# Performance work log

Measured on AMD Instinct MI355X. Metric: run time of the kernel, lower is better.

The kernel has to match this reference:

```python
import jax, jax.numpy as jnp
import numpy as np

MESH_SIZE = 0.01
TEMP = 0.001
T = 4096
HID = (16, 16, 16)


def _triangle_mesh():
    g = np.arange(-1.0, 1.0 + 1e-9, MESH_SIZE, dtype=np.float32)  # 201 pts
    A, B = np.meshgrid(g, g, indexing='ij')  # alpha rows, beta cols
    mask = A >= B                             # Preisach triangle alpha >= beta
    return A[mask].astype(np.float32), B[mask].astype(np.float32)  # [N], [N]


def _constrain(v, lo, hi):
    return lo + (hi - lo) * jax.nn.sigmoid(v)


def setup_inputs() -> dict:
    key = jax.random.key(0)
    ks = jax.random.split(key, 12)
    alpha_np, beta_np = _triangle_mesh()
    N = alpha_np.shape[0]  # 20301

    def xavier(k, fan_in, fan_out):
        b = np.sqrt(6.0 / (fan_in + fan_out)).astype(np.float32)
        return jax.random.uniform(k, (fan_in, fan_out), jnp.float32, -b, b)

    dims = (2,) + HID + (1,)
    params = {}
    for i in range(4):
        params[f'w{i+1}'] = xavier(ks[i], dims[i], dims[i + 1])
        params[f'b{i+1}'] = jnp.zeros((dims[i + 1],), jnp.float32)

    bound = np.sqrt(6.0 / (1 + N)).astype(np.float32)  # xavier_uniform on (1,N)
    init_state_raw = jax.random.uniform(ks[10], (N,), jnp.float32, -bound, bound)

    return dict(
        x=jax.random.normal(ks[11], (T,), jnp.float32),
        alpha_raw=jnp.asarray(alpha_np),
        beta_raw=jnp.asarray(beta_np),
        init_state_raw=init_state_raw,
        m_scale_raw=jnp.asarray(1.0, jnp.float32),
        m_offset_raw=jnp.asarray(1.0, jnp.float32),
        h_scale_raw=jnp.asarray(1.0, jnp.float32),
        **params,
    )


def _get_states(x, alpha, beta, s0, temp):
    # Soft Preisach relay: switch up where u>alpha, down where u<beta, else hold.
    def step(s, u):
        up = jax.nn.sigmoid((u - alpha) / temp)
        dn = jax.nn.sigmoid((beta - u) / temp)
        s_new = up - dn + (1.0 - up) * (1.0 - dn) * s
        return s_new, s_new
    _, states = jax.lax.scan(step, s0, x)
    return states  # [T, N]


def reference(x, alpha_raw, beta_raw, init_state_raw,
              w1, b1, w2, b2, w3, b3, w4, b4,
              m_scale_raw, m_offset_raw, h_scale_raw):
    alpha = alpha_raw  # ConstrainedParameter with no bounds -> identity
    beta = beta_raw
    s0 = jnp.tanh(init_state_raw)  # BinaryParameter (soft binary)

    states = _get_states(x, alpha, beta, s0, TEMP)  # [T, N]

    mesh = jnp.stack([alpha, beta], axis=1)  # [N, 2]
    h = jax.nn.relu(mesh @ w1 + b1)
    h = jax.nn.relu(h @ w2 + b2)
    h = jax.nn.relu(h @ w3 + b3)
    density = jax.nn.sigmoid(h @ w4 + b4)  # [N, 1]
    density = density.T  # [1, N]

    m = jnp.sum(density * states, axis=-1) / jnp.sum(density, axis=-1)  # [T]

    m_scale = _constrain(m_scale_raw, 0.0, 10.0)
    m_offset = _constrain(m_offset_raw, -10.0, 10.0)
    h_scale = _constrain(h_scale_raw, 0.0, 10.0)

    out = m_scale * m + m_offset + h_scale * x  # [T]
    return out, density, states
```

## Files before the change

### kernel.cpp

```cpp
#include <hip/hip_runtime.h>
#include <math.h>

#define NM 20301
#define TT 4096
#define NC 16
#define CH 256
#define NBLK 80
#define NWAVE 4
#define NPAR (NBLK*NWAVE)
#define TPH 16
#define NPH (CH / TPH)
#define LOG2E_K 1442.69504f

__device__ __forceinline__ void relay_step(float ka, float kb, float ku,
                                           float& aa, float& bb) {
    float z1 = fminf(ka - ku, 63.f);
    float z2 = fminf(ku - kb, 63.f);
    float e1 = __builtin_amdgcn_exp2f(z1);
    float e2 = __builtin_amdgcn_exp2f(z2);
    float p1 = 1.f + e1, p2 = 1.f + e2;
    float r  = __builtin_amdgcn_rcpf(p1 * p2);
    aa = (e2 - e1) * r;
    bb = (e1 * e2) * r;
}

__device__ __forceinline__ float wave_reduce_sum(float w) {
    #pragma unroll
    for (int off = 32; off > 0; off >>= 1)
        w += __shfl_down(w, off, 64);
    return w;
}

__global__ __launch_bounds__(256) void density_kernel(
    const float* __restrict__ alpha, const float* __restrict__ beta,
    const float* __restrict__ w1, const float* __restrict__ b1,
    const float* __restrict__ w2, const float* __restrict__ b2,
    const float* __restrict__ w3, const float* __restrict__ b3,
    const float* __restrict__ w4, const float* __restrict__ b4,
    float* __restrict__ density_out, float* __restrict__ densum_parts)
{
    int n = blockIdx.x * 256 + threadIdx.x;
    bool valid = n < NM;
    int nn = valid ? n : NM - 1;
    float a = alpha[nn], b = beta[nn];

    float h1[16], h2[16], h3[16];
    #pragma unroll
    for (int j = 0; j < 16; j++) {
        float v = fmaf(a, w1[j], fmaf(b, w1[16 + j], b1[j]));
        h1[j] = fmaxf(v, 0.f);
    }
    #pragma unroll
    for (int j = 0; j < 16; j++) {
        float v = b2[j];
        #pragma unroll
        for (int k = 0; k < 16; k++) v = fmaf(h1[k], w2[k * 16 + j], v);
        h2[j] = fmaxf(v, 0.f);
    }
    #pragma unroll
    for (int j = 0; j < 16; j++) {
        float v = b3[j];
        #pragma unroll
        for (int k = 0; k < 16; k++) v = fmaf(h2[k], w3[k * 16 + j], v);
        h3[j] = fmaxf(v, 0.f);
    }
    float v = b4[0];
    #pragma unroll
    for (int k = 0; k < 16; k++) v = fmaf(h3[k], w4[k], v);
    float d = 1.f / (1.f + __expf(-v));

    if (valid) density_out[n] = d;
    float wsum = wave_reduce_sum(valid ? d : 0.f);
    __shared__ float ws_[NWAVE];
    if ((threadIdx.x & 63) == 0) ws_[threadIdx.x >> 6] = wsum;
    __syncthreads();
    if (threadIdx.x == 0)
        densum_parts[blockIdx.x] = ws_[0] + ws_[1] + ws_[2] + ws_[3];
}

__global__ __launch_bounds__(256) void chunk_compose_kernel(
    const float* __restrict__ x, const float* __restrict__ alpha,
    const float* __restrict__ beta,
    float* __restrict__ Abuf, float* __restrict__ Bbuf)
{
    __shared__ float xs[CH];
    int c = blockIdx.y;
    xs[threadIdx.x] = x[c * CH + threadIdx.x] * LOG2E_K;
    __syncthreads();

    int n = blockIdx.x * 256 + threadIdx.x;
    int nn = (n < NM) ? n : NM - 1;
    float ka = alpha[nn] * LOG2E_K;
    float kb = beta[nn] * LOG2E_K;

    float A = 0.f, B = 1.f;
    #pragma unroll 8
    for (int i = 0; i < CH; i++) {
        float aa, bb;
        relay_step(ka, kb, xs[i], aa, bb);
        A = fmaf(bb, A, aa);
        B *= bb;
    }
    if (n < NM) { Abuf[c * NM + n] = A; Bbuf[c * NM + n] = B; }
}

__global__ __launch_bounds__(256) void chunk_scan_kernel(
    const float* __restrict__ init_raw,
    const float* __restrict__ Abuf, const float* __restrict__ Bbuf,
    float* __restrict__ sstart)
{
    int n = blockIdx.x * 256 + threadIdx.x;
    if (n >= NM) return;
    float s = tanhf(init_raw[n]);
    #pragma unroll
    for (int c = 0; c < NC; c++) {
        sstart[c * NM + n] = s;
        s = fmaf(Bbuf[c * NM + n], s, Abuf[c * NM + n]);
    }
}

__global__ __launch_bounds__(256) void states_kernel(
    const float* __restrict__ x, const float* __restrict__ alpha,
    const float* __restrict__ beta, const float* __restrict__ density,
    const float* __restrict__ sstart,
    float* __restrict__ states, float* __restrict__ partials)
{
    __shared__ float xs[CH];
    __shared__ float tile[NWAVE * 64 * (TPH + 1)];

    int tid = threadIdx.x;
    int c = blockIdx.y;
    xs[tid] = x[c * CH + tid] * LOG2E_K;

    int n = blockIdx.x * 256 + tid;
    bool valid = n < NM;
    int nn = valid ? n : NM - 1;
    float ka = alpha[nn] * LOG2E_K;
    float kb = beta[nn] * LOG2E_K;
    float d  = valid ? density[n] : 0.f;
    float s  = sstart[c * NM + nn];
    __syncthreads();

    int wv = tid >> 6, ln = tid & 63;
    int tl = ln & 15, h = ln >> 4;
    float* wtile = &tile[wv * 64 * (TPH + 1)];
    float* tslot = &wtile[ln * (TPH + 1)];
    float* rowp  = states + (size_t)c * CH * NM + n;
    size_t prow  = (size_t)(blockIdx.x * NWAVE + wv) * TT + c * CH;

    for (int p = 0; p < NPH; p++) {
        #pragma unroll
        for (int j = 0; j < TPH; j++) {
            int i = p * TPH + j;
            float aa, bb;
            relay_step(ka, kb, xs[i], aa, bb);
            s = fmaf(bb, s, aa);
            if (valid) __builtin_nontemporal_store(s, rowp + (size_t)i * NM);
            tslot[j] = d * s;
        }
        asm volatile("s_waitcnt lgkmcnt(0)" ::: "memory");
        float acc = 0.f;
        #pragma unroll
        for (int k = 0; k < TPH; k++)
            acc += wtile[(h * 16 + k) * (TPH + 1) + tl];
        acc += __shfl_xor(acc, 16, 64);
        acc += __shfl_xor(acc, 32, 64);
        if (ln < TPH) partials[prow + p * TPH + ln] = acc;
        asm volatile("s_waitcnt lgkmcnt(0)" ::: "memory");
    }
}

__global__ __launch_bounds__(256) void finalize_kernel(
    const float* __restrict__ x, const float* __restrict__ partials,
    const float* __restrict__ densum_parts,
    const float* __restrict__ msr, const float* __restrict__ mor,
    const float* __restrict__ hsr, float* __restrict__ out)
{
    int t = blockIdx.x * 256 + threadIdx.x;
    if (t >= TT) return;
    float acc = 0.f;
    for (int r = 0; r < NPAR; r++)
        acc += partials[(size_t)r * TT + t];
    float dsum = 0.f;
    for (int bx = 0; bx < NBLK; bx++)
        dsum += densum_parts[bx];
    float sig_ms = 1.f / (1.f + __expf(-msr[0]));
    float sig_mo = 1.f / (1.f + __expf(-mor[0]));
    float sig_hs = 1.f / (1.f + __expf(-hsr[0]));
    float m_scale  = 10.f * sig_ms;
    float m_offset = fmaf(20.f, sig_mo, -10.f);
    float h_scale  = 10.f * sig_hs;
    float m = acc / dsum;
    out[t] = fmaf(m_scale, m, m_offset) + h_scale * x[t];
}

extern "C" void kernel_launch(void* const* d_in, const int* in_sizes, int n_in,
                              void* d_out, int out_size, void* d_ws, size_t ws_size,
                              hipStream_t stream)
{
    const float* x    = (const float*)d_in[0];
    const float* alpha= (const float*)d_in[1];
    const float* beta = (const float*)d_in[2];
    const float* init = (const float*)d_in[3];
    const float* msr  = (const float*)d_in[4];
    const float* mor  = (const float*)d_in[5];
    const float* hsr  = (const float*)d_in[6];
    const float* w1   = (const float*)d_in[7];
    const float* b1   = (const float*)d_in[8];
    const float* w2   = (const float*)d_in[9];
    const float* b2   = (const float*)d_in[10];
    const float* w3   = (const float*)d_in[11];
    const float* b3   = (const float*)d_in[12];
    const float* w4   = (const float*)d_in[13];
    const float* b4   = (const float*)d_in[14];

    float* out     = (float*)d_out;
    float* density = out + TT;
    float* states  = density + NM;

    float* densum_parts = (float*)d_ws;
    float* sstart       = densum_parts + 128;
    float* partials     = sstart + NC * NM;

    float* Abuf = states;
    float* Bbuf = states + (size_t)NC * NM;

    density_kernel<<<dim3(NBLK), dim3(256), 0, stream>>>(
        alpha, beta, w1, b1, w2, b2, w3, b3, w4, b4, density, densum_parts);

    chunk_compose_kernel<<<dim3(NBLK, NC), dim3(256), 0, stream>>>(
        x, alpha, beta, Abuf, Bbuf);

    chunk_scan_kernel<<<dim3(NBLK), dim3(256), 0, stream>>>(
        init, Abuf, Bbuf, sstart);

    states_kernel<<<dim3(NBLK, NC), dim3(256), 0, stream>>>(
        x, alpha, beta, density, sstart, states, partials);

    finalize_kernel<<<dim3(TT / 256), dim3(256), 0, stream>>>(
        x, partials, densum_parts, msr, mor, hsr, out);
}
```

Baseline: 512.4 us.

## Fuse pipeline into cooperative mega-kernel with saturated-relay fast path

Replaces the five launches with one cooperative kernel that uses grid.sync between phases: density MLP plus chunk composition, then states with an inline chunk-prefix scan, then the final reduction. Adds a wave-uniform branch that skips the exp/rcp relay math when every lane's input is far from both thresholds, setting the saturated value directly. Also drops the nontemporal stores and switches to 64-wide per-wave tasks with 8-step partial sums. It removes launch overhead and transcendental work, at the cost of grid-sync overhead, the redundant prefix recompute and a branch that only pays off when inputs are often saturated.

```diff
diff --git a/kernel.cpp b/kernel.cpp
--- a/kernel.cpp
+++ b/kernel.cpp
@@ -1,16 +1,20 @@
 #include <hip/hip_runtime.h>
+#include <hip/hip_cooperative_groups.h>
 #include <math.h>
+
+namespace cg = cooperative_groups;
 
 #define NM 20301
 #define TT 4096
 #define NC 16
 #define CH 256
-#define NBLK 80
-#define NWAVE 4
-#define NPAR (NBLK*NWAVE)
-#define TPH 16
-#define NPH (CH / TPH)
+#define NW 318
+#define NMP (NW * 64)
+#define NTASK (NW * NC)
+#define NBLOCKS 256
+#define NTH 1024
 #define LOG2E_K 1442.69504f
+#define WNEAR 26.0f
 
 __device__ __forceinline__ void relay_step(float ka, float kb, float ku,
                                            float& aa, float& bb) {
@@ -31,167 +35,167 @@
     return w;
 }
 
-__global__ __launch_bounds__(256) void density_kernel(
-    const float* __restrict__ alpha, const float* __restrict__ beta,
+__global__ __launch_bounds__(NTH, 4) void mega_kernel(
+    const float* __restrict__ x, const float* __restrict__ alpha,
+    const float* __restrict__ beta, const float* __restrict__ init_raw,
+    const float* __restrict__ msr, const float* __restrict__ mor,
+    const float* __restrict__ hsr,
     const float* __restrict__ w1, const float* __restrict__ b1,
     const float* __restrict__ w2, const float* __restrict__ b2,
     const float* __restrict__ w3, const float* __restrict__ b3,
     const float* __restrict__ w4, const float* __restrict__ b4,
-    float* __restrict__ density_out, float* __restrict__ densum_parts)
+    float* __restrict__ out, float* __restrict__ density,
+    float* __restrict__ states,
+    float* __restrict__ Ag, float* __restrict__ Bg,
+    float* __restrict__ wpart, float* __restrict__ s0g,
+    float* __restrict__ dparts)
 {
-    int n = blockIdx.x * 256 + threadIdx.x;
-    bool valid = n < NM;
-    int nn = valid ? n : NM - 1;
-    float a = alpha[nn], b = beta[nn];
-
-    float h1[16], h2[16], h3[16];
+    __shared__ float xall[TT];
+    __shared__ float tiles[16 * 64 * 9];
+
+    cg::grid_group grid = cg::this_grid();
+    int b = blockIdx.x, tid = threadIdx.x;
+    int ln = tid & 63, wv = tid >> 6;
+    int g = b * NTH + tid;
+
+    for (int q = tid; q < TT; q += NTH) xall[q] = x[q] * LOG2E_K;
+    __syncthreads();
+
+    if (g < NMP) {
+        bool valid = g < NM;
+        int nn = valid ? g : NM - 1;
+        float a = alpha[nn], bb_ = beta[nn];
+        float h1[16], h2[16], h3[16];
+        #pragma unroll
+        for (int j = 0; j < 16; j++) {
+            float v = fmaf(a, w1[j], fmaf(bb_, w1[16 + j], b1[j]));
+            h1[j] = fmaxf(v, 0.f);
+        }
+        #pragma unroll
+        for (int j = 0; j < 16; j++) {
+            float v = b2[j];
+            #pragma unroll
+            for (int k = 0; k < 16; k++) v = fmaf(h1[k], w2[k * 16 + j], v);
+            h2[j] = fmaxf(v, 0.f);
+        }
+        #pragma unroll
+        for (int j = 0; j < 16; j++) {
+            float v = b3[j];
+            #pragma unroll
+            for (int k = 0; k < 16; k++) v = fmaf(h2[k], w3[k * 16 + j], v);
+            h3[j] = fmaxf(v, 0.f);
+        }
+        float v = b4[0];
+        #pragma unroll
+        for (int k = 0; k < 16; k++) v = fmaf(h3[k], w4[k], v);
+        float d = 1.f / (1.f + __expf(-v));
+        if (valid) { density[g] = d; s0g[g] = tanhf(init_raw[g]); }
+        float wsum = wave_reduce_sum(valid ? d : 0.f);
+        if (ln == 0) dparts[g >> 6] = wsum;
+    }
+
     #pragma unroll
-    for (int j = 0; j < 16; j++) {
-        float v = fmaf(a, w1[j], fmaf(b, w1[16 + j], b1[j]));
-        h1[j] = fmaxf(v, 0.f);
-    }
-    #pragma unroll
-    for (int j = 0; j < 16; j++) {
-        float v = b2[j];
-        #pragma unroll
-        for (int k = 0; k < 16; k++) v = fmaf(h1[k], w2[k * 16 + j], v);
-        h2[j] = fmaxf(v, 0.f);
-    }
-    #pragma unroll
-    for (int j = 0; j < 16; j++) {
-        float v = b3[j];
-        #pragma unroll
-        for (int k = 0; k < 16; k++) v = fmaf(h2[k], w3[k * 16 + j], v);
-        h3[j] = fmaxf(v, 0.f);
-    }
-    float v = b4[0];
-    #pragma unroll
-    for (int k = 0; k < 16; k++) v = fmaf(h3[k], w4[k], v);
-    float d = 1.f / (1.f + __expf(-v));
-
-    if (valid) density_out[n] = d;
-    float wsum = wave_reduce_sum(valid ? d : 0.f);
-    __shared__ float ws_[NWAVE];
-    if ((threadIdx.x & 63) == 0) ws_[threadIdx.x >> 6] = wsum;
-    __syncthreads();
-    if (threadIdx.x == 0)
-        densum_parts[blockIdx.x] = ws_[0] + ws_[1] + ws_[2] + ws_[3];
-}
-
-__global__ __launch_bounds__(256) void chunk_compose_kernel(
-    const float* __restrict__ x, const float* __restrict__ alpha,
-    const float* __restrict__ beta,
-    float* __restrict__ Abuf, float* __restrict__ Bbuf)
-{
-    __shared__ float xs[CH];
-    int c = blockIdx.y;
-    xs[threadIdx.x] = x[c * CH + threadIdx.x] * LOG2E_K;
-    __syncthreads();
-
-    int n = blockIdx.x * 256 + threadIdx.x;
-    int nn = (n < NM) ? n : NM - 1;
-    float ka = alpha[nn] * LOG2E_K;
-    float kb = beta[nn] * LOG2E_K;
-
-    float A = 0.f, B = 1.f;
-    #pragma unroll 8
-    for (int i = 0; i < CH; i++) {
-        float aa, bb;
-        relay_step(ka, kb, xs[i], aa, bb);
-        A = fmaf(bb, A, aa);
-        B *= bb;
-    }
-    if (n < NM) { Abuf[c * NM + n] = A; Bbuf[c * NM + n] = B; }
-}
-
-__global__ __launch_bounds__(256) void chunk_scan_kernel(
-    const float* __restrict__ init_raw,
-    const float* __restrict__ Abuf, const float* __restrict__ Bbuf,
-    float* __restrict__ sstart)
-{
-    int n = blockIdx.x * 256 + threadIdx.x;
-    if (n >= NM) return;
-    float s = tanhf(init_raw[n]);
-    #pragma unroll
-    for (int c = 0; c < NC; c++) {
-        sstart[c * NM + n] = s;
-        s = fmaf(Bbuf[c * NM + n], s, Abuf[c * NM + n]);
-    }
-}
-
-__global__ __launch_bounds__(256) void states_kernel(
-    const float* __restrict__ x, const float* __restrict__ alpha,
-    const float* __restrict__ beta, const float* __restrict__ density,
-    const float* __restrict__ sstart,
-    float* __restrict__ states, float* __restrict__ partials)
-{
-    __shared__ float xs[CH];
-    __shared__ float tile[NWAVE * 64 * (TPH + 1)];
-
-    int tid = threadIdx.x;
-    int c = blockIdx.y;
-    xs[tid] = x[c * CH + tid] * LOG2E_K;
-
-    int n = blockIdx.x * 256 + tid;
-    bool valid = n < NM;
-    int nn = valid ? n : NM - 1;
-    float ka = alpha[nn] * LOG2E_K;
-    float kb = beta[nn] * LOG2E_K;
-    float d  = valid ? density[n] : 0.f;
-    float s  = sstart[c * NM + nn];
-    __syncthreads();
-
-    int wv = tid >> 6, ln = tid & 63;
-    int tl = ln & 15, h = ln >> 4;
-    float* wtile = &tile[wv * 64 * (TPH + 1)];
-    float* tslot = &wtile[ln * (TPH + 1)];
-    float* rowp  = states + (size_t)c * CH * NM + n;
-    size_t prow  = (size_t)(blockIdx.x * NWAVE + wv) * TT + c * CH;
-
-    for (int p = 0; p < NPH; p++) {
-        #pragma unroll
-        for (int j = 0; j < TPH; j++) {
-            int i = p * TPH + j;
-            float aa, bb;
-            relay_step(ka, kb, xs[i], aa, bb);
-            s = fmaf(bb, s, aa);
-            if (valid) __builtin_nontemporal_store(s, rowp + (size_t)i * NM);
-            tslot[j] = d * s;
-        }
-        asm volatile("s_waitcnt lgkmcnt(0)" ::: "memory");
+    for (int rep = 0; rep < 2; rep++) {
+        int idx = g + rep * (NBLOCKS * NTH);
+        if (idx < NC * NMP) {
+            int c = idx / NMP;
+            int n = idx - c * NMP;
+            int nn = (n < NM) ? n : NM - 1;
+            float ka = alpha[nn] * LOG2E_K;
+            float kb = beta[nn] * LOG2E_K;
+            float A = 0.f, Bv = 1.f;
+            const float* xc = &xall[c * CH];
+            #pragma unroll 8
+            for (int i = 0; i < CH; i++) {
+                float u = xc[i];
+                float d1 = ka - u, d2 = u - kb;
+                bool nearb = fminf(fabsf(d1), fabsf(d2)) < WNEAR;
+                if (__any(nearb)) {
+                    float aa, bb;
+                    relay_step(ka, kb, u, aa, bb);
+                    A = fmaf(bb, A, aa);
+                    Bv *= bb;
+                } else {
+                    bool su = d1 < 0.f, sd = d2 < 0.f;
+                    A  = su ? 1.f : (sd ? -1.f : A);
+                    Bv = (su || sd) ? 0.f : Bv;
+                }
+            }
+            if (n < NM) { Ag[c * NM + n] = A; Bg[c * NM + n] = Bv; }
+        }
+    }
+
+    grid.sync();
+
+    {
+        int t0 = (b * NTASK) >> 8;
+        int t1 = ((b + 1) * NTASK) >> 8;
+        float* wt = &tiles[wv * 576];
+        float* ts = &wt[ln * 9];
+        int tl = ln & 7, g8 = ln >> 3;
+        for (int w = t0 + wv; w < t1; w += 16) {
+            int c = w / NW, nblk = w - c * NW;
+            int n = nblk * 64 + ln;
+            bool valid = n < NM;
+            int nn = valid ? n : NM - 1;
+            float ka = alpha[nn] * LOG2E_K;
+            float kb = beta[nn] * LOG2E_K;
+            float d  = valid ? density[nn] : 0.f;
+            float s  = s0g[nn];
+            for (int cc = 0; cc < c; cc++)
+                s = fmaf(Bg[cc * NM + nn], s, Ag[cc * NM + nn]);
+            const float* xc = &xall[c * CH];
+            float* rowp = states + (size_t)c * CH * NM + n;
+            size_t wp = (size_t)w * CH;
+            for (int p = 0; p < 32; p++) {
+                #pragma unroll
+                for (int j = 0; j < 8; j++) {
+                    int i = p * 8 + j;
+                    float u = xc[i];
+                    float d1 = ka - u, d2 = u - kb;
+                    bool nearb = fminf(fabsf(d1), fabsf(d2)) < WNEAR;
+                    if (__any(nearb)) {
+                        float aa, bb;
+                        relay_step(ka, kb, u, aa, bb);
+                        s = fmaf(bb, s, aa);
+                    } else {
+                        s = (d1 < 0.f) ? 1.f : ((d2 < 0.f) ? -1.f : s);
+                    }
+                    if (valid) rowp[(size_t)i * NM] = s;
+                    ts[j] = d * s;
+                }
+                asm volatile("s_waitcnt lgkmcnt(0)" ::: "memory");
+                float acc = 0.f;
+                #pragma unroll
+                for (int k = 0; k < 8; k++)
+                    acc += wt[(g8 * 8 + k) * 9 + tl];
+                acc += __shfl_xor(acc, 8, 64);
+                acc += __shfl_xor(acc, 16, 64);
+                acc += __shfl_xor(acc, 32, 64);
+                if (ln < 8) wpart[wp + p * 8 + ln] = acc;
+                asm volatile("s_waitcnt lgkmcnt(0)" ::: "memory");
+            }
+        }
+    }
+
+    grid.sync();
+
+    if (g < TT) {
+        int c = g >> 8, i = g & 255;
         float acc = 0.f;
-        #pragma unroll
-        for (int k = 0; k < TPH; k++)
-            acc += wtile[(h * 16 + k) * (TPH + 1) + tl];
-        acc += __shfl_xor(acc, 16, 64);
-        acc += __shfl_xor(acc, 32, 64);
-        if (ln < TPH) partials[prow + p * TPH + ln] = acc;
-        asm volatile("s_waitcnt lgkmcnt(0)" ::: "memory");
-    }
-}
-
-__global__ __launch_bounds__(256) void finalize_kernel(
-    const float* __restrict__ x, const float* __restrict__ partials,
-    const float* __restrict__ densum_parts,
-    const float* __restrict__ msr, const float* __restrict__ mor,
-    const float* __restrict__ hsr, float* __restrict__ out)
-{
-    int t = blockIdx.x * 256 + threadIdx.x;
-    if (t >= TT) return;
-    float acc = 0.f;
-    for (int r = 0; r < NPAR; r++)
-        acc += partials[(size_t)r * TT + t];
-    float dsum = 0.f;
-    for (int bx = 0; bx < NBLK; bx++)
-        dsum += densum_parts[bx];
-    float sig_ms = 1.f / (1.f + __expf(-msr[0]));
-    float sig_mo = 1.f / (1.f + __expf(-mor[0]));
-    float sig_hs = 1.f / (1.f + __expf(-hsr[0]));
-    float m_scale  = 10.f * sig_ms;
-    float m_offset = fmaf(20.f, sig_mo, -10.f);
-    float h_scale  = 10.f * sig_hs;
-    float m = acc / dsum;
-    out[t] = fmaf(m_scale, m, m_offset) + h_scale * x[t];
+        for (int nb = 0; nb < NW; nb++)
+            acc += wpart[((size_t)(c * NW + nb)) * CH + i];
+        float dsum = 0.f;
+        for (int nb = 0; nb < NW; nb++) dsum += dparts[nb];
+        float sig_ms = 1.f / (1.f + __expf(-msr[0]));
+        float sig_mo = 1.f / (1.f + __expf(-mor[0]));
+        float sig_hs = 1.f / (1.f + __expf(-hsr[0]));
+        float m_scale  = 10.f * sig_ms;
+        float m_offset = fmaf(20.f, sig_mo, -10.f);
+        float h_scale  = 10.f * sig_hs;
+        float m = acc / dsum;
+        out[g] = fmaf(m_scale, m, m_offset) + h_scale * x[g];
+    }
 }
 
 extern "C" void kernel_launch(void* const* d_in, const int* in_sizes, int n_in,
@@ -218,25 +222,20 @@
     float* density = out + TT;
     float* states  = density + NM;
 
-    float* densum_parts = (float*)d_ws;
-    float* sstart       = densum_parts + 128;
-    float* partials     = sstart + NC * NM;
-
-    float* Abuf = states;
-    float* Bbuf = states + (size_t)NC * NM;
-
-    density_kernel<<<dim3(NBLK), dim3(256), 0, stream>>>(
-        alpha, beta, w1, b1, w2, b2, w3, b3, w4, b4, density, densum_parts);
-
-    chunk_compose_kernel<<<dim3(NBLK, NC), dim3(256), 0, stream>>>(
-        x, alpha, beta, Abuf, Bbuf);
-
-    chunk_scan_kernel<<<dim3(NBLK), dim3(256), 0, stream>>>(
-        init, Abuf, Bbuf, sstart);
-
-    states_kernel<<<dim3(NBLK, NC), dim3(256), 0, stream>>>(
-        x, alpha, beta, density, sstart, states, partials);
-
-    finalize_kernel<<<dim3(TT / 256), dim3(256), 0, stream>>>(
-        x, partials, densum_parts, msr, mor, hsr, out);
-}
+    float* Ag     = (float*)d_ws;
+    float* Bg     = Ag + NC * NM;
+    float* wpart  = Bg + NC * NM;
+    float* s0g    = wpart + (size_t)NTASK * CH;
+    float* dparts = s0g + NM + 64;
+
+    void* args[] = {
+        (void*)&x, (void*)&alpha, (void*)&beta, (void*)&init,
+        (void*)&msr, (void*)&mor, (void*)&hsr,
+        (void*)&w1, (void*)&b1, (void*)&w2, (void*)&b2,
+        (void*)&w3, (void*)&b3, (void*)&w4, (void*)&b4,
+        (void*)&out, (void*)&density, (void*)&states,
+        (void*)&Ag, (void*)&Bg, (void*)&wpart, (void*)&s0g, (void*)&dparts
+    };
+    hipLaunchCooperativeKernel((void*)mega_kernel, dim3(NBLOCKS), dim3(NTH),
+                               args, 0, stream);
+}
```

Result: slower. 595.5 us (+16.2%).
